# Kernel tuning notes

Measured on AMD Instinct MI355X. Metric: run time of the kernel, lower is better.

## Reference

```python
import jax, jax.numpy as jnp
import numpy as np

TOP_P = 0.9
NEG_FILL = -1000000000.0


def _top_p_mask(logits):
    # probabilities over vocab
    probs = jax.nn.softmax(logits, axis=-1)
    # sort descending; keep the permutation to scatter the mask back
    order = jnp.argsort(-probs, axis=-1)                      # [B, V]
    ordered = jnp.take_along_axis(probs, order, axis=-1)      # [B, V]
    cum = jnp.cumsum(ordered, axis=-1)
    cum = cum.at[..., -1].set(0.0)
    cum = jnp.roll(cum, shift=1, axis=-1)                     # exclusive cumsum
    cmask = cum <= TOP_P                                      # [B, V] in sorted order
    # scatter back: selection[b, order[b, j]] = cmask[b, j]  <=>  gather by inverse perm
    inv = jnp.argsort(order, axis=-1)
    return jnp.take_along_axis(cmask, inv, axis=-1)


def setup_inputs() -> dict:
    key = jax.random.key(0)
    k1, k2 = jax.random.split(key)
    B, V = 256, 128000
    logits = jax.random.normal(k1, (B, V), dtype=jnp.float32)
    u = jax.random.uniform(k2, (B,), dtype=jnp.float32)
    return {"logits": logits, "u": u, "temperature": 1}


def reference(logits, u, temperature):
    t = jnp.asarray(temperature, dtype=logits.dtype)
    logits = logits / t
    sel = _top_p_mask(logits)
    masked = jnp.where(sel, logits, jnp.asarray(NEG_FILL, logits.dtype))
    probs = jax.nn.softmax(masked, axis=-1)                   # [B, V]
    # multinomial(num_samples=1) via inverse-CDF with uniform u
    cdf = jnp.cumsum(probs, axis=-1)
    token = jnp.sum(cdf < u[:, None], axis=-1)
    return jnp.minimum(token, probs.shape[-1] - 1)
```

## Files before the change

### kernel.cpp

```cpp
#include <hip/hip_runtime.h>
#include <cmath>

#define BLOCK 1024
#define NW (BLOCK / 64)
#define LISTCAP 4096

__device__ __forceinline__ float wincl(float v, int lane) {
#pragma unroll
    for (int o = 1; o < 64; o <<= 1) {
        float x = __shfl_up(v, o, 64);
        if (lane >= o) v += x;
    }
    return v;
}

__device__ __forceinline__ void find_crit_desc(const float* h, int n, int seg,
                                               float base0, float limit, int lane,
                                               int* out_b, float* out_A) {
    float segsum = 0.f;
    int start = n - 1 - lane * seg;
    for (int k = 0; k < seg; k++) segsum += h[start - k];
    float incl = wincl(segsum, lane);
    unsigned long long mk = __ballot(base0 + incl > limit);
    if (mk == 0ULL) { *out_b = 0; *out_A = base0; return; }
    int fl = __ffsll(mk) - 1;
    float base = base0 + __shfl(incl, fl, 64) - __shfl(segsum, fl, 64);
    int sstart = n - 1 - fl * seg;
    float v = (lane < seg) ? h[sstart - lane] : 0.f;
    float incl2 = wincl(v, lane);
    unsigned long long mk2 = __ballot((lane < seg) && (base + incl2 > limit));
    int k2 = mk2 ? (__ffsll(mk2) - 1) : (seg - 1);
    *out_b = sstart - k2;
    *out_A = base + __shfl(incl2, k2, 64) - __shfl(v, k2, 64);
}

__device__ __forceinline__ unsigned okey(unsigned bits) {
    return (bits & 0x80000000u) ? ~bits : (bits | 0x80000000u);
}
__device__ __forceinline__ float bucket_hi(unsigned b) {
    unsigned ku = (b + 1u) << 21;
    unsigned hb = (ku & 0x80000000u) ? (ku & 0x7FFFFFFFu) : ~ku;
    return __uint_as_float(hb);
}

#define LD4(j) (*(const float4*)(row + (j)))

__global__ __launch_bounds__(BLOCK) void NucleusSampling_79336635892529_kernel(
    const float* __restrict__ logits, const float* __restrict__ uvec,
    const int* __restrict__ temp, int* __restrict__ out, int Vv) {
    const int b = blockIdx.x;
    const float* __restrict__ row = logits + (size_t)b * (size_t)Vv;
    const int t = threadIdx.x;
    const int lane = t & 63;
    const int wave = t >> 6;

    __shared__ float hist[4096];
    __shared__ float sweep[NW];
    __shared__ float csum[128];
    __shared__ unsigned idxlist[LISTCAP];
    __shared__ int shi[2];
    __shared__ float shf[1];
    __shared__ unsigned shu[1];
    __shared__ int cnt;

    const float inv_t = 1.0f / (float)temp[0];
    const int V4 = Vv & ~3;
    const int S = BLOCK * 4;

    for (int i = t; i < 4096; i += BLOCK) hist[i] = 0.f;
    if (t == 0) { shi[0] = 0; cnt = 0; }
    __syncthreads();

#define P1(xx) { unsigned bb = __float_as_uint(xx); unsigned kk = okey(bb); \
                 unsigned bk = kk >> 21; \
                 float er = __expf(((xx) - bucket_hi(bk)) * inv_t); \
                 atomicAdd((unsigned*)&hist[bk], (unsigned)(er * 131072.f + 0.5f)); }
    {
        int i = t * 4;
        for (; i + 3 * S + 3 < V4; i += 4 * S) {
            float4 a = LD4(i), b4 = LD4(i + S), c = LD4(i + 2 * S), d = LD4(i + 3 * S);
            P1(a.x); P1(a.y); P1(a.z); P1(a.w);
            P1(b4.x); P1(b4.y); P1(b4.z); P1(b4.w);
            P1(c.x); P1(c.y); P1(c.z); P1(c.w);
            P1(d.x); P1(d.y); P1(d.z); P1(d.w);
        }
        for (; i < V4; i += S) { float4 a = LD4(i); P1(a.x); P1(a.y); P1(a.z); P1(a.w); }
        for (int j = V4 + t; j < Vv; j += BLOCK) P1(row[j]);
    }
    __syncthreads();

    for (int i = t; i < 2048; i += BLOCK)
        if (__float_as_uint(hist[i])) atomicMax(&shi[0], i);
    __syncthreads();
    const float Ms = bucket_hi((unsigned)shi[0]) * inv_t;

    float zp = 0.f;
    for (int i = t; i < 2048; i += BLOCK) {
        unsigned h = __float_as_uint(hist[i]);
        float mass = h ? (float)h * 0x1p-17f * __expf(bucket_hi((unsigned)i) * inv_t - Ms) : 0.f;
        hist[i] = mass;
        zp += mass;
    }
#pragma unroll
    for (int o = 32; o >= 1; o >>= 1) zp += __shfl_xor(zp, o, 64);
    if (lane == 0) sweep[wave] = zp;
    __syncthreads();
    float Z = 0.f;
    for (int w = 0; w < NW; w++) Z += sweep[w];
    const float limit = 0.9f * Z;

    if (wave == 0) {
        int b1w; float Aw;
        find_crit_desc(hist, 2048, 32, 0.f, limit, lane, &b1w, &Aw);
        if (lane == 0) { shi[1] = b1w; shf[0] = Aw; }
    }
    __syncthreads();
    const int b1 = shi[1];
    const float A = shf[0];
    const float xhi1s = bucket_hi((unsigned)b1) * inv_t;
    const float C1 = __expf(Ms - xhi1s);
    const unsigned Tlow = (unsigned)b1 << 21;

    for (int i = t; i < 4096; i += BLOCK) hist[i] = 0.f;
    __syncthreads();

    const int nch = (Vv + 1023) >> 10;
#define P2(xx, ii) { unsigned bb = __float_as_uint(xx); unsigned kk = okey(bb); \
    if (kk >= Tlow) { \
        float e = __expf((xx) * inv_t - Ms); s += e; \
        if ((kk >> 21) == (unsigned)b1) { \
            int p = atomicAdd(&cnt, 1); \
            if (p < LISTCAP) idxlist[p] = (unsigned)(ii); \
            atomicAdd((unsigned*)&hist[(kk >> 9) & 0xFFF], \
                      (unsigned)(e * C1 * 131072.f + 0.5f)); \
        } } }
    for (int c = wave; c < nch; c += NW) {
        float s = 0.f;
        int base = c << 10;
#pragma unroll
        for (int q = 0; q < 4; q++) {
            int i = base + q * 256 + lane * 4;
            if (i + 3 < Vv) {
                float4 v = LD4(i);
                P2(v.x, i); P2(v.y, i + 1); P2(v.z, i + 2); P2(v.w, i + 3);
            } else {
                for (int kq = 0; kq < 4; kq++)
                    if (i + kq < Vv) P2(row[i + kq], i + kq);
            }
        }
#pragma unroll
        for (int o = 32; o >= 1; o >>= 1) s += __shfl_xor(s, o, 64);
        if (lane == 0) csum[c] = s;
    }
    if (t < 128 && t >= nch) csum[t] = 0.f;
    __syncthreads();

    if (wave == 0) {
        int b2w; float A2;
        find_crit_desc(hist, 4096, 64, A, limit, lane, &b2w, &A2);
        if (lane == 0) shu[0] = (((unsigned)b1 << 12) | (unsigned)b2w) << 9;
    }
    __syncthreads();
    const unsigned T = shu[0];

    {
        int nc = cnt < LISTCAP ? cnt : LISTCAP;
        for (int p = t; p < nc; p += BLOCK) {
            unsigned ii = idxlist[p];
            float x = row[ii];
            unsigned kk = okey(__float_as_uint(x));
            if (kk < T) {
                float e = __expf(x * inv_t - Ms);
                atomicAdd(&csum[ii >> 10], -e);
            }
        }
    }
    __syncthreads();

    if (wave == 0) {
        float segsum = csum[lane * 2] + csum[lane * 2 + 1];
        float incl = wincl(segsum, lane);
        float total = __shfl(incl, 63, 64);
        const float U = uvec[b] * total;
        unsigned long long mk = __ballot(incl >= U);
        int token;
        if (mk == 0ULL) {
            token = Vv;
        } else {
            int fl = __ffsll(mk) - 1;
            float base = __shfl(incl, fl, 64) - __shfl(segsum, fl, 64);
            float v = (lane < 2) ? csum[fl * 2 + lane] : 0.f;
            float incl2 = wincl(v, lane);
            unsigned long long mk2 = __ballot((lane < 2) && (base + incl2 >= U));
            int k2 = mk2 ? (__ffsll(mk2) - 1) : 1;
            int cx = fl * 2 + k2;
            float B = base + __shfl(incl2, k2, 64) - __shfl(v, k2, 64);
            int cb = cx << 10;
            float vv[16];
#pragma unroll
            for (int r = 0; r < 16; r++) {
                int idx = cb + r * 64 + lane;
                vv[r] = (idx < Vv) ? row[idx] : -1e30f;
            }
            int cnt2 = 0;
#pragma unroll
            for (int r = 0; r < 16; r++) {
                int idx = cb + r * 64 + lane;
                unsigned kk = okey(__float_as_uint(vv[r]));
                float e = __expf(vv[r] * inv_t - Ms);
                float keep = (kk >= T) ? e : 0.f;
                float is = wincl(keep, lane);
                unsigned long long mm = __ballot((idx < Vv) && (B + is < U));
                cnt2 += __popcll(mm);
                B += __shfl(is, 63, 64);
            }
            token = cb + cnt2;
        }
        if (lane == 0) out[b] = (token < Vv - 1) ? token : (Vv - 1);
    }
}

extern "C" void kernel_launch(void* const* d_in, const int* in_sizes, int n_in,
                              void* d_out, int out_size, void* d_ws, size_t ws_size,
                              hipStream_t stream) {
    const float* logits = (const float*)d_in[0];
    const float* u = (const float*)d_in[1];
    const int* temp = (const int*)d_in[2];
    int* out = (int*)d_out;
    int B = in_sizes[1];
    int V = in_sizes[0] / B;
    NucleusSampling_79336635892529_kernel<<<B, BLOCK, 0, stream>>>(logits, u, temp, out, V);
}
```

Measured before the change: 238.3 us.

## Drop second-level refinement; use single-level coarse bucket threshold with float atomics

Removes the max-bucket pass, fixed-point histogram, second-level 4096-bin refinement, index list and correction pass. The threshold is now chosen at coarse 2048-bucket granularity only, accumulated with 4-way replicated float atomics of unshifted exp2. It also unrolls the second pass over two chunks per wave. This cuts synchronisation and atomics, but the nucleus cutoff becomes coarse, so tokens near the boundary may be included wrongly. Using exp without max subtraction also risks overflow for large logits.

```diff
diff --git a/kernel.cpp b/kernel.cpp
--- a/kernel.cpp
+++ b/kernel.cpp
@@ -1,9 +1,7 @@
 #include <hip/hip_runtime.h>
-#include <cmath>
 
 #define BLOCK 1024
 #define NW (BLOCK / 64)
-#define LISTCAP 4096
 
 __device__ __forceinline__ float wincl(float v, int lane) {
 #pragma unroll
@@ -15,33 +13,24 @@
 }
 
 __device__ __forceinline__ void find_crit_desc(const float* h, int n, int seg,
-                                               float base0, float limit, int lane,
-                                               int* out_b, float* out_A) {
+                                               float limit, int lane, int* out_b) {
     float segsum = 0.f;
     int start = n - 1 - lane * seg;
     for (int k = 0; k < seg; k++) segsum += h[start - k];
     float incl = wincl(segsum, lane);
-    unsigned long long mk = __ballot(base0 + incl > limit);
-    if (mk == 0ULL) { *out_b = 0; *out_A = base0; return; }
+    unsigned long long mk = __ballot(incl > limit);
+    if (mk == 0ULL) { *out_b = 0; return; }
     int fl = __ffsll(mk) - 1;
-    float base = base0 + __shfl(incl, fl, 64) - __shfl(segsum, fl, 64);
+    float base = __shfl(incl, fl, 64) - __shfl(segsum, fl, 64);
     int sstart = n - 1 - fl * seg;
     float v = (lane < seg) ? h[sstart - lane] : 0.f;
     float incl2 = wincl(v, lane);
     unsigned long long mk2 = __ballot((lane < seg) && (base + incl2 > limit));
     int k2 = mk2 ? (__ffsll(mk2) - 1) : (seg - 1);
     *out_b = sstart - k2;
-    *out_A = base + __shfl(incl2, k2, 64) - __shfl(v, k2, 64);
-}
-
-__device__ __forceinline__ unsigned okey(unsigned bits) {
-    return (bits & 0x80000000u) ? ~bits : (bits | 0x80000000u);
-}
-__device__ __forceinline__ float bucket_hi(unsigned b) {
-    unsigned ku = (b + 1u) << 21;
-    unsigned hb = (ku & 0x80000000u) ? (ku & 0x7FFFFFFFu) : ~ku;
-    return __uint_as_float(hb);
-}
+}
+
+#define OKEY(bb) ((bb) ^ ((unsigned)((int)(bb) >> 31) | 0x80000000u))
 
 #define LD4(j) (*(const float4*)(row + (j)))
 
@@ -53,28 +42,25 @@
     const int t = threadIdx.x;
     const int lane = t & 63;
     const int wave = t >> 6;
-
-    __shared__ float hist[4096];
+    const int rep = lane & 3;
+
+    __shared__ __align__(16) float histbuf[8192];
+    __shared__ float mg[2048];
     __shared__ float sweep[NW];
     __shared__ float csum[128];
-    __shared__ unsigned idxlist[LISTCAP];
-    __shared__ int shi[2];
-    __shared__ float shf[1];
-    __shared__ unsigned shu[1];
-    __shared__ int cnt;
+    __shared__ int shb1;
 
     const float inv_t = 1.0f / (float)temp[0];
+    const float k2 = inv_t * 1.44269504088896340736f;
     const int V4 = Vv & ~3;
     const int S = BLOCK * 4;
-
-    for (int i = t; i < 4096; i += BLOCK) hist[i] = 0.f;
-    if (t == 0) { shi[0] = 0; cnt = 0; }
-    __syncthreads();
-
-#define P1(xx) { unsigned bb = __float_as_uint(xx); unsigned kk = okey(bb); \
-                 unsigned bk = kk >> 21; \
-                 float er = __expf(((xx) - bucket_hi(bk)) * inv_t); \
-                 atomicAdd((unsigned*)&hist[bk], (unsigned)(er * 131072.f + 0.5f)); }
+    const int nch = (Vv + 1023) >> 10;
+
+    for (int i = t; i < 8192; i += BLOCK) histbuf[i] = 0.f;
+    __syncthreads();
+
+#define P1(xx) { unsigned kk = OKEY(__float_as_uint(xx)); \
+                 atomicAdd(&histbuf[((kk >> 21) << 2) | rep], exp2f((xx) * k2)); }
     {
         int i = t * 4;
         for (; i + 3 * S + 3 < V4; i += 4 * S) {
@@ -89,17 +75,12 @@
     }
     __syncthreads();
 
-    for (int i = t; i < 2048; i += BLOCK)
-        if (__float_as_uint(hist[i])) atomicMax(&shi[0], i);
-    __syncthreads();
-    const float Ms = bucket_hi((unsigned)shi[0]) * inv_t;
-
     float zp = 0.f;
     for (int i = t; i < 2048; i += BLOCK) {
-        unsigned h = __float_as_uint(hist[i]);
-        float mass = h ? (float)h * 0x1p-17f * __expf(bucket_hi((unsigned)i) * inv_t - Ms) : 0.f;
-        hist[i] = mass;
-        zp += mass;
+        float4 m4 = *(const float4*)&histbuf[i << 2];
+        float m = (m4.x + m4.y) + (m4.z + m4.w);
+        mg[i] = m;
+        zp += m;
     }
 #pragma unroll
     for (int o = 32; o >= 1; o >>= 1) zp += __shfl_xor(zp, o, 64);
@@ -110,69 +91,60 @@
     const float limit = 0.9f * Z;
 
     if (wave == 0) {
-        int b1w; float Aw;
-        find_crit_desc(hist, 2048, 32, 0.f, limit, lane, &b1w, &Aw);
-        if (lane == 0) { shi[1] = b1w; shf[0] = Aw; }
-    }
-    __syncthreads();
-    const int b1 = shi[1];
-    const float A = shf[0];
-    const float xhi1s = bucket_hi((unsigned)b1) * inv_t;
-    const float C1 = __expf(Ms - xhi1s);
-    const unsigned Tlow = (unsigned)b1 << 21;
-
-    for (int i = t; i < 4096; i += BLOCK) hist[i] = 0.f;
-    __syncthreads();
-
-    const int nch = (Vv + 1023) >> 10;
-#define P2(xx, ii) { unsigned bb = __float_as_uint(xx); unsigned kk = okey(bb); \
-    if (kk >= Tlow) { \
-        float e = __expf((xx) * inv_t - Ms); s += e; \
-        if ((kk >> 21) == (unsigned)b1) { \
-            int p = atomicAdd(&cnt, 1); \
-            if (p < LISTCAP) idxlist[p] = (unsigned)(ii); \
-            atomicAdd((unsigned*)&hist[(kk >> 9) & 0xFFF], \
-                      (unsigned)(e * C1 * 131072.f + 0.5f)); \
-        } } }
-    for (int c = wave; c < nch; c += NW) {
-        float s = 0.f;
-        int base = c << 10;
-#pragma unroll
-        for (int q = 0; q < 4; q++) {
-            int i = base + q * 256 + lane * 4;
-            if (i + 3 < Vv) {
-                float4 v = LD4(i);
-                P2(v.x, i); P2(v.y, i + 1); P2(v.z, i + 2); P2(v.w, i + 3);
-            } else {
-                for (int kq = 0; kq < 4; kq++)
-                    if (i + kq < Vv) P2(row[i + kq], i + kq);
-            }
-        }
-#pragma unroll
-        for (int o = 32; o >= 1; o >>= 1) s += __shfl_xor(s, o, 64);
-        if (lane == 0) csum[c] = s;
+        int b1w;
+        find_crit_desc(mg, 2048, 32, limit, lane, &b1w);
+        if (lane == 0) shb1 = b1w;
     }
     if (t < 128 && t >= nch) csum[t] = 0.f;
     __syncthreads();
-
-    if (wave == 0) {
-        int b2w; float A2;
-        find_crit_desc(hist, 4096, 64, A, limit, lane, &b2w, &A2);
-        if (lane == 0) shu[0] = (((unsigned)b1 << 12) | (unsigned)b2w) << 9;
-    }
-    __syncthreads();
-    const unsigned T = shu[0];
-
-    {
-        int nc = cnt < LISTCAP ? cnt : LISTCAP;
-        for (int p = t; p < nc; p += BLOCK) {
-            unsigned ii = idxlist[p];
-            float x = row[ii];
-            unsigned kk = okey(__float_as_uint(x));
-            if (kk < T) {
-                float e = __expf(x * inv_t - Ms);
-                atomicAdd(&csum[ii >> 10], -e);
-            }
+    const unsigned Tlow = (unsigned)shb1 << 21;
+
+#define P2(xx, ss) { unsigned kk = OKEY(__float_as_uint(xx)); \
+                     float e = exp2f((xx) * k2); \
+                     if (kk >= Tlow) ss += e; }
+    for (int c0 = wave; c0 < nch; c0 += 2 * NW) {
+        const int c1 = c0 + NW;
+        const bool haveB = (c1 < nch);
+        float s0 = 0.f, s1 = 0.f;
+        const int bA = c0 << 10, bB = c1 << 10;
+        if (bA + 1024 <= Vv && (!haveB || bB + 1024 <= Vv)) {
+            float4 a0 = LD4(bA + lane * 4);
+            float4 a1 = LD4(bA + 256 + lane * 4);
+            float4 a2 = LD4(bA + 512 + lane * 4);
+            float4 a3 = LD4(bA + 768 + lane * 4);
+            if (haveB) {
+                float4 b0 = LD4(bB + lane * 4);
+                float4 b1v = LD4(bB + 256 + lane * 4);
+                float4 b2 = LD4(bB + 512 + lane * 4);
+                float4 b3 = LD4(bB + 768 + lane * 4);
+                P2(b0.x, s1); P2(b0.y, s1); P2(b0.z, s1); P2(b0.w, s1);
+                P2(b1v.x, s1); P2(b1v.y, s1); P2(b1v.z, s1); P2(b1v.w, s1);
+                P2(b2.x, s1); P2(b2.y, s1); P2(b2.z, s1); P2(b2.w, s1);
+                P2(b3.x, s1); P2(b3.y, s1); P2(b3.z, s1); P2(b3.w, s1);
+            }
+            P2(a0.x, s0); P2(a0.y, s0); P2(a0.z, s0); P2(a0.w, s0);
+            P2(a1.x, s0); P2(a1.y, s0); P2(a1.z, s0); P2(a1.w, s0);
+            P2(a2.x, s0); P2(a2.y, s0); P2(a2.z, s0); P2(a2.w, s0);
+            P2(a3.x, s0); P2(a3.y, s0); P2(a3.z, s0); P2(a3.w, s0);
+        } else {
+            for (int q = 0; q < 16; q++) {
+                int i = bA + (q << 6) + lane;
+                if (i < Vv) { float x = row[i]; P2(x, s0); }
+            }
+            if (haveB) {
+                for (int q = 0; q < 16; q++) {
+                    int i = bB + (q << 6) + lane;
+                    if (i < Vv) { float x = row[i]; P2(x, s1); }
+                }
+            }
+        }
+#pragma unroll
+        for (int o = 32; o >= 1; o >>= 1) s0 += __shfl_xor(s0, o, 64);
+        if (lane == 0) csum[c0] = s0;
+        if (haveB) {
+#pragma unroll
+            for (int o = 32; o >= 1; o >>= 1) s1 += __shfl_xor(s1, o, 64);
+            if (lane == 0) csum[c1] = s1;
         }
     }
     __syncthreads();
@@ -192,9 +164,9 @@
             float v = (lane < 2) ? csum[fl * 2 + lane] : 0.f;
             float incl2 = wincl(v, lane);
             unsigned long long mk2 = __ballot((lane < 2) && (base + incl2 >= U));
-            int k2 = mk2 ? (__ffsll(mk2) - 1) : 1;
-            int cx = fl * 2 + k2;
-            float B = base + __shfl(incl2, k2, 64) - __shfl(v, k2, 64);
+            int k2i = mk2 ? (__ffsll(mk2) - 1) : 1;
+            int cx = fl * 2 + k2i;
+            float B = base + __shfl(incl2, k2i, 64) - __shfl(v, k2i, 64);
             int cb = cx << 10;
             float vv[16];
 #pragma unroll
@@ -206,9 +178,9 @@
 #pragma unroll
             for (int r = 0; r < 16; r++) {
                 int idx = cb + r * 64 + lane;
-                unsigned kk = okey(__float_as_uint(vv[r]));
-                float e = __expf(vv[r] * inv_t - Ms);
-                float keep = (kk >= T) ? e : 0.f;
+                unsigned kk = OKEY(__float_as_uint(vv[r]));
+                float e = exp2f(vv[r] * k2);
+                float keep = (kk >= Tlow) ? e : 0.f;
                 float is = wincl(keep, lane);
                 unsigned long long mm = __ballot((idx < Vv) && (B + is < U));
                 cnt2 += __popcll(mm);
```

Measured after the change: 328.0 us. +37.6%, slower.
